# Kernel optimization log

Hardware: AMD Instinct MI355X
Metric: run time of the kernel (lower is better)

## Reference

```python
import jax, jax.numpy as jnp
import numpy as np

NUM_EXPERTS = 8
TOP_K = 2
B, L, H = 4, 4096, 1024


def setup_inputs() -> dict:
    key = jax.random.key(0)
    ks = jax.random.split(key, 5)
    s = 1.0 / np.sqrt(H)
    return {
        "hidden_states": jax.random.normal(ks[0], (B, L, H), dtype=jnp.float32),
        "gate_w": jax.random.normal(ks[1], (H, NUM_EXPERTS), dtype=jnp.float32) * s,
        "w1": jax.random.normal(ks[2], (NUM_EXPERTS, H, 2 * H), dtype=jnp.float32) * s,
        "b1": jnp.zeros((NUM_EXPERTS, 2 * H), dtype=jnp.float32),
        "w2": jax.random.normal(ks[3], (NUM_EXPERTS, 2 * H, H), dtype=jnp.float32) * (1.0 / np.sqrt(2 * H)),
        "b2": jnp.zeros((NUM_EXPERTS, H), dtype=jnp.float32),
    }


def reference(hidden_states, gate_w, w1, b1, w2, b2):
    b, l, h = hidden_states.shape
    flat = hidden_states.reshape(-1, h)                      # [T, H]
    router_logits = flat @ gate_w                            # [T, E]
    probs = jax.nn.softmax(router_logits, axis=-1)
    weights, indices = jax.lax.top_k(probs, TOP_K)           # [T, K]
    weights = weights / jnp.sum(weights, axis=-1, keepdims=True)
    # combine[t, e] = sum_k weights[t, k] * 1{indices[t, k] == e}
    onehot = jax.nn.one_hot(indices, NUM_EXPERTS, dtype=flat.dtype)  # [T, K, E]
    combine = jnp.einsum('tk,tke->te', weights, onehot)      # [T, E]
    out = jnp.zeros_like(flat)
    for e in range(NUM_EXPERTS):  # fixed small expert loop; dense-compute, sparse-combine
        hdn = jax.nn.relu(flat @ w1[e] + b1[e])              # [T, 2H]
        y = hdn @ w2[e] + b2[e]                              # [T, H]
        out = out + combine[:, e:e + 1] * y
    return out.reshape(b, l, h)
```

## Files before the change

kernel.cpp:

```cpp
#include <hip/hip_runtime.h>
#include <hip/hip_bf16.h>
#include <stdint.h>

#define T_TOK 16384
#define HD    1024
#define HD2   2048
#define NE    8
#define ROWS  (2*T_TOK)
#define MAXT  264
#define RTOK  32

#define M_NT    256
#define M_OFFS  272
#define M_TILES 288

typedef __bf16 bf16x8 __attribute__((ext_vector_type(8)));
typedef float f32x4 __attribute__((ext_vector_type(4)));
typedef float f32x16 __attribute__((ext_vector_type(16)));

#define GLD16(g, l) __builtin_amdgcn_global_load_lds( \
    (const __attribute__((address_space(1))) void*)(g), \
    (__attribute__((address_space(3))) void*)(l), 16, 0, 0)

__device__ inline unsigned short f2bf(float f) {
    unsigned int u = __float_as_uint(f);
    unsigned int r = (u + 0x7fffu + ((u >> 16) & 1u)) >> 16;
    return (unsigned short)r;
}

__global__ __launch_bounds__(256) void cvt_wT(const float* __restrict__ w,
                                              unsigned short* __restrict__ wt,
                                              int K, int N) {
    __shared__ float t[32][33];
    int e = blockIdx.z;
    int n0 = blockIdx.x * 32, k0 = blockIdx.y * 32;
    int r = threadIdx.x >> 3;
    int c4 = (threadIdx.x & 7) * 4;
    const float* src = w + ((size_t)e * K + k0 + r) * N + n0 + c4;
    float4 v = *(const float4*)src;
    t[r][c4] = v.x; t[r][c4+1] = v.y; t[r][c4+2] = v.z; t[r][c4+3] = v.w;
    __syncthreads();
    int cc = threadIdx.x & 7;
    ushort4 o;
    o.x = f2bf(t[cc*4+0][r]); o.y = f2bf(t[cc*4+1][r]);
    o.z = f2bf(t[cc*4+2][r]); o.w = f2bf(t[cc*4+3][r]);
    *(ushort4*)(wt + ((size_t)e * N + n0 + r) * K + k0 + cc*4) = o;
}

__global__ __launch_bounds__(256) void router_k(const float* __restrict__ x,
        const float* __restrict__ gw, int* __restrict__ meta,
        int* __restrict__ tok_e, int* __restrict__ tok_slot, float* __restrict__ tok_w,
        unsigned short* __restrict__ xb) {
    __shared__ float g[NE * HD];
    __shared__ int   le[RTOK * 2];
    __shared__ float lw[RTOK * 2];
    __shared__ int   lslot[RTOK * 2];
    __shared__ int   lcnt[NE];
    __shared__ int   lbase[NE];
    for (int i = threadIdx.x; i < NE * HD; i += 256) {
        int k = i >> 3, e = i & 7;
        g[e * HD + k] = gw[i];
    }
    if (threadIdx.x < NE) lcnt[threadIdx.x] = 0;
    __syncthreads();

    int wave = threadIdx.x >> 6, lane = threadIdx.x & 63;
    int t0 = blockIdx.x * RTOK;
    for (int i = 0; i < RTOK / 4; i++) {
        int tt = wave * (RTOK / 4) + i;
        int t = t0 + tt;
        const float4* xr = (const float4*)(x + (size_t)t * HD);
        float acc[NE];
#pragma unroll
        for (int e = 0; e < NE; e++) acc[e] = 0.f;
#pragma unroll
        for (int j = 0; j < HD / 256; j++) {
            float4 xv = xr[lane + 64 * j];
            ushort4 o4;
            o4.x = f2bf(xv.x); o4.y = f2bf(xv.y);
            o4.z = f2bf(xv.z); o4.w = f2bf(xv.w);
            *(ushort4*)(xb + (size_t)t * HD + (lane + 64 * j) * 4) = o4;
#pragma unroll
            for (int e = 0; e < NE; e++) {
                float4 gv = *(const float4*)&g[e * HD + (lane + 64 * j) * 4];
                acc[e] += xv.x * gv.x + xv.y * gv.y + xv.z * gv.z + xv.w * gv.w;
            }
        }
#pragma unroll
        for (int e = 0; e < NE; e++) {
            float v = acc[e];
#pragma unroll
            for (int off = 32; off > 0; off >>= 1) v += __shfl_down(v, off, 64);
            acc[e] = v;
        }
        if (lane == 0) {
            int e1 = 0; float l1 = acc[0];
#pragma unroll
            for (int e = 1; e < NE; e++) if (acc[e] > l1) { l1 = acc[e]; e1 = e; }
            int e2 = -1; float l2 = -3.0e38f;
#pragma unroll
            for (int e = 0; e < NE; e++) if (e != e1 && acc[e] > l2) { l2 = acc[e]; e2 = e; }
            float w1 = 1.f / (1.f + expf(l2 - l1));
            le[tt * 2] = e1;     le[tt * 2 + 1] = e2;
            lw[tt * 2] = w1;     lw[tt * 2 + 1] = 1.f - w1;
        }
    }
    __syncthreads();
    if (threadIdx.x < RTOK * 2)
        lslot[threadIdx.x] = atomicAdd(&lcnt[le[threadIdx.x]], 1);
    __syncthreads();
    if (threadIdx.x < NE)
        lbase[threadIdx.x] = atomicAdd(&meta[threadIdx.x * 32], lcnt[threadIdx.x]);
    __syncthreads();
    if (threadIdx.x < RTOK * 2) {
        int gi = t0 * 2 + threadIdx.x;
        int e = le[threadIdx.x];
        tok_e[gi]    = e;
        tok_slot[gi] = lbase[e] + lslot[threadIdx.x];
        tok_w[gi]    = lw[threadIdx.x];
    }
}

__global__ __launch_bounds__(64) void offsets_k(int* __restrict__ meta) {
    int lane = threadIdx.x;
    int cl = (lane < NE) ? meta[lane * 32] : 0;
    int cnt[NE], offs[NE], tbase[NE];
    int o = 0, tb = 0;
#pragma unroll
    for (int e = 0; e < NE; e++) {
        cnt[e] = __shfl(cl, e, 64);
        offs[e] = o;  o += cnt[e];
        tbase[e] = tb; tb += (cnt[e] + 127) >> 7;
    }
    int nt = tb;
    if (lane == 0) meta[M_NT] = nt;
    if (lane < NE) meta[M_OFFS + lane] = offs[lane];
    for (int i = lane; i < nt; i += 64) {
        int e = 0;
#pragma unroll
        for (int k = 1; k < NE; k++) if (i >= tbase[k]) e = k;
        int m = i - tbase[e];
        int r0 = offs[e] + m * 128;
        int re = offs[e] + cnt[e];
        if (r0 + 128 < re) re = r0 + 128;
        meta[M_TILES + i] = e;
        meta[M_TILES + MAXT + i] = r0;
        meta[M_TILES + 2 * MAXT + i] = re;
    }
}

__global__ __launch_bounds__(256) void scatter_k(const int* __restrict__ meta,
        const int* __restrict__ tok_e, const int* __restrict__ tok_slot,
        const float* __restrict__ tok_w, int* __restrict__ rows_tok,
        float* __restrict__ rows_w) {
    int i = blockIdx.x * 256 + threadIdx.x;
    const int* offs = meta + M_OFFS;
    int e = tok_e[i];
    int r = offs[e] + tok_slot[i];
    rows_tok[r] = i >> 1;
    rows_w[r] = tok_w[i];
}

__global__ __launch_bounds__(256) void gemm1_k(
    const unsigned short* __restrict__ Xbf,
    const unsigned short* __restrict__ W1T,
    const float* __restrict__ b1,
    const int* __restrict__ meta,
    const int* __restrict__ rows_tok,
    unsigned short* __restrict__ hdn)
{
    __shared__ unsigned short As[128 * 64];
    __shared__ unsigned short Bs[128 * 64];
    int nt = meta[M_NT];
    int mt = blockIdx.y;
    if (mt >= nt) return;
    int e    = meta[M_TILES + mt];
    int r0   = meta[M_TILES + MAXT + mt];
    int rend = meta[M_TILES + 2 * MAXT + mt];
    int n0 = blockIdx.x * 128;

    int tid = threadIdx.x, w = tid >> 6, lane = tid & 63;

    const unsigned short* srcA[4];
    const unsigned short* srcB[4];
#pragma unroll
    for (int j = 0; j < 4; j++) {
        int g = w * 256 + j * 64 + lane;
        int row = g >> 3;
        int c = (g & 7) ^ (row & 7);
        int grow = r0 + row; grow = grow < ROWS - 1 ? grow : ROWS - 1;
        int tok = rows_tok[grow];
        srcA[j] = Xbf + (size_t)tok * HD + c * 8;
        srcB[j] = W1T + ((size_t)e * HD2 + n0 + row) * HD + c * 8;
    }
    int wm = (w & 1) * 64, wn = (w >> 1) * 64;

    f32x4 acc[4][4];
#pragma unroll
    for (int a = 0; a < 4; a++)
#pragma unroll
        for (int b = 0; b < 4; b++) acc[a][b] = (f32x4){0.f, 0.f, 0.f, 0.f};

    for (int kt = 0; kt < HD / 64; kt++) {
        __syncthreads();
#pragma unroll
        for (int j = 0; j < 4; j++) {
            GLD16(srcA[j] + kt * 64, &As[(w * 256 + j * 64) * 8]);
            GLD16(srcB[j] + kt * 64, &Bs[(w * 256 + j * 64) * 8]);
        }
        __syncthreads();
#pragma unroll
        for (int s = 0; s < 2; s++) {
            bf16x8 af[4], bfr[4];
            int q = lane >> 4, cA = s * 4 + q;
#pragma unroll
            for (int i = 0; i < 4; i++) {
                int rowA = wm + i * 16 + (lane & 15);
                af[i] = *(const bf16x8*)&As[(rowA * 8 + (cA ^ (rowA & 7))) * 8];
                int rowB = wn + i * 16 + (lane & 15);
                bfr[i] = *(const bf16x8*)&Bs[(rowB * 8 + (cA ^ (rowB & 7))) * 8];
            }
#pragma unroll
            for (int im = 0; im < 4; im++)
#pragma unroll
                for (int in = 0; in < 4; in++)
                    acc[im][in] = __builtin_amdgcn_mfma_f32_16x16x32_bf16(
                        af[im], bfr[in], acc[im][in], 0, 0, 0);
        }
    }

    const float* b1e = b1 + (size_t)e * HD2 + n0 + wn;
    int q = lane >> 4;
#pragma unroll
    for (int in = 0; in < 4; in++) {
        float bias = b1e[in * 16 + (lane & 15)];
#pragma unroll
        for (int im = 0; im < 4; im++) {
            int rbase = r0 + wm + im * 16 + q * 4;
#pragma unroll
            for (int i = 0; i < 4; i++) {
                int r = rbase + i;
                if (r < rend) {
                    float v = acc[im][in][i] + bias;
                    v = v > 0.f ? v : 0.f;
                    hdn[(size_t)r * HD2 + n0 + wn + in * 16 + (lane & 15)] = f2bf(v);
                }
            }
        }
    }
}

__global__ __launch_bounds__(256) void gemm2_k(
    const unsigned short* __restrict__ hdn,
    const unsigned short* __restrict__ W2T,
    const float* __restrict__ b2,
    const int* __restrict__ meta,
    const int* __restrict__ rows_tok,
    const float* __restrict__ rows_w,
    float* __restrict__ out)
{
    __shared__ unsigned short As[128 * 64];
    __shared__ unsigned short Bs[128 * 64];
    int nt = meta[M_NT];
    int mt = blockIdx.y;
    if (mt >= nt) return;
    int e    = meta[M_TILES + mt];
    int r0   = meta[M_TILES + MAXT + mt];
    int rend = meta[M_TILES + 2 * MAXT + mt];
    int n0 = blockIdx.x * 128;

    int tid = threadIdx.x, w = tid >> 6, lane = tid & 63;

    const unsigned short* srcA[4];
    const unsigned short* srcB[4];
#pragma unroll
    for (int j = 0; j < 4; j++) {
        int g = w * 256 + j * 64 + lane;
        int row = g >> 3;
        int c = (g & 7) ^ (row & 7);
        int grow = r0 + row; grow = grow < ROWS - 1 ? grow : ROWS - 1;
        srcA[j] = hdn + (size_t)grow * HD2 + c * 8;
        srcB[j] = W2T + ((size_t)e * HD + n0 + row) * HD2 + c * 8;
    }
    int wm = (w & 1) * 64, wn = (w >> 1) * 64;

    f32x16 acc[2][2];
#pragma unroll
    for (int a = 0; a < 2; a++)
#pragma unroll
        for (int b = 0; b < 2; b++)
#pragma unroll
            for (int i = 0; i < 16; i++) acc[a][b][i] = 0.f;

    int kh = lane >> 5;
    int rl = lane & 31;
    for (int kt = 0; kt < HD2 / 64; kt++) {
        __syncthreads();
#pragma unroll
        for (int j = 0; j < 4; j++) {
            GLD16(srcA[j] + kt * 64, &As[(w * 256 + j * 64) * 8]);
            GLD16(srcB[j] + kt * 64, &Bs[(w * 256 + j * 64) * 8]);
        }
        __syncthreads();
#pragma unroll
        for (int s = 0; s < 4; s++) {
            int c = s * 2 + kh;
            bf16x8 af[2], bfr[2];
#pragma unroll
            for (int i = 0; i < 2; i++) {
                int rowA = wm + i * 32 + rl;
                af[i] = *(const bf16x8*)&As[(rowA * 8 + (c ^ (rowA & 7))) * 8];
                int rowB = wn + i * 32 + rl;
                bfr[i] = *(const bf16x8*)&Bs[(rowB * 8 + (c ^ (rowB & 7))) * 8];
            }
#pragma unroll
            for (int im = 0; im < 2; im++)
#pragma unroll
                for (int in = 0; in < 2; in++)
                    acc[im][in] = __builtin_amdgcn_mfma_f32_32x32x16_bf16(
                        af[im], bfr[in], acc[im][in], 0, 0, 0);
        }
    }

    int col = lane & 31;
    float bias0 = b2[(size_t)e * HD + n0 + wn + col];
    float bias1 = b2[(size_t)e * HD + n0 + wn + 32 + col];
#pragma unroll
    for (int im = 0; im < 2; im++) {
        int rb = r0 + wm + im * 32 + 4 * kh;
#pragma unroll
        for (int g = 0; g < 4; g++) {
            int toks[4]; float wgts[4];
#pragma unroll
            for (int t = 0; t < 4; t++) {
                int r = rb + 8 * g + t;
                int rc = r < ROWS - 1 ? r : ROWS - 1;
                toks[t] = rows_tok[rc];
                wgts[t] = rows_w[rc];
            }
#pragma unroll
            for (int in = 0; in < 2; in++) {
                float bias = in ? bias1 : bias0;
#pragma unroll
                for (int t = 0; t < 4; t++) {
                    int r = rb + 8 * g + t;
                    if (r < rend) {
                        float v = (acc[im][in][g * 4 + t] + bias) * wgts[t];
                        atomicAdd(&out[(size_t)toks[t] * HD + n0 + wn + in * 32 + col], v);
                    }
                }
            }
        }
    }
}

extern "C" void kernel_launch(void* const* d_in, const int* in_sizes, int n_in,
                              void* d_out, int out_size, void* d_ws, size_t ws_size,
                              hipStream_t stream) {
    const float* x  = (const float*)d_in[0];
    const float* gw = (const float*)d_in[1];
    const float* w1 = (const float*)d_in[2];
    const float* b1 = (const float*)d_in[3];
    const float* w2 = (const float*)d_in[4];
    const float* b2 = (const float*)d_in[5];
    float* out = (float*)d_out;

    uint8_t* ws = (uint8_t*)d_ws;
    unsigned short* Xbf = (unsigned short*)(ws);
    unsigned short* W1T = (unsigned short*)(ws + 33554432ull);
    unsigned short* W2T = (unsigned short*)(ws + 67108864ull);
    unsigned short* HDN = (unsigned short*)(ws + 100663296ull);
    int*   meta     = (int*)(ws + 234881024ull);
    int*   tok_e    = meta + 2048;
    int*   tok_slot = tok_e + ROWS;
    float* tok_w    = (float*)(tok_slot + ROWS);
    int*   rows_tok = (int*)(tok_w + ROWS);
    float* rows_w   = (float*)(rows_tok + ROWS);

    hipMemsetAsync(meta, 0, 1024, stream);
    hipMemsetAsync(d_out, 0, (size_t)out_size * sizeof(float), stream);

    cvt_wT<<<dim3(HD2 / 32, HD / 32, NE), 256, 0, stream>>>(w1, W1T, HD, HD2);
    cvt_wT<<<dim3(HD / 32, HD2 / 32, NE), 256, 0, stream>>>(w2, W2T, HD2, HD);
    router_k<<<T_TOK / RTOK, 256, 0, stream>>>(x, gw, meta, tok_e, tok_slot, tok_w, Xbf);
    offsets_k<<<1, 64, 0, stream>>>(meta);
    scatter_k<<<ROWS / 256, 256, 0, stream>>>(meta, tok_e, tok_slot, tok_w, rows_tok, rows_w);
    gemm1_k<<<dim3(HD2 / 128, MAXT), 256, 0, stream>>>(Xbf, W1T, b1, meta, rows_tok, HDN);
    gemm2_k<<<dim3(HD / 128, MAXT), 256, 0, stream>>>(HDN, W2T, b2, meta, rows_tok, rows_w, out);
}
```

Measured before the change: 773.5 us.

## Use 256x256 tiles with double-buffered LDS pipelining in both expert GEMMs

Both grouped GEMMs move from 128x128 tiles with 256 threads to 256x256 tiles with 512 threads and 8 waves. The main loop now double-buffers LDS and interleaves async global-to-LDS loads of the next k-tile with MFMA on the current one, using explicit waitcnt, barriers and setprio. Block indices are remapped so consecutive blocks share weight tiles, and routing tiles become 256 rows. This aims to hide memory latency and raise data reuse, at the cost of 128KB LDS per block, heavier register pressure and more padding waste on partial expert tiles.

```diff
diff --git a/kernel.cpp b/kernel.cpp
--- a/kernel.cpp
+++ b/kernel.cpp
@@ -8,6 +8,7 @@
 #define NE    8
 #define ROWS  (2*T_TOK)
 #define MAXT  264
+#define MT256 136
 #define RTOK  32
 
 #define M_NT    256
@@ -16,7 +17,6 @@
 
 typedef __bf16 bf16x8 __attribute__((ext_vector_type(8)));
 typedef float f32x4 __attribute__((ext_vector_type(4)));
-typedef float f32x16 __attribute__((ext_vector_type(16)));
 
 #define GLD16(g, l) __builtin_amdgcn_global_load_lds( \
     (const __attribute__((address_space(1))) void*)(g), \
@@ -130,7 +130,7 @@
     for (int e = 0; e < NE; e++) {
         cnt[e] = __shfl(cl, e, 64);
         offs[e] = o;  o += cnt[e];
-        tbase[e] = tb; tb += (cnt[e] + 127) >> 7;
+        tbase[e] = tb; tb += (cnt[e] + 255) >> 8;
     }
     int nt = tb;
     if (lane == 0) meta[M_NT] = nt;
@@ -140,9 +140,9 @@
 #pragma unroll
         for (int k = 1; k < NE; k++) if (i >= tbase[k]) e = k;
         int m = i - tbase[e];
-        int r0 = offs[e] + m * 128;
+        int r0 = offs[e] + m * 256;
         int re = offs[e] + cnt[e];
-        if (r0 + 128 < re) re = r0 + 128;
+        if (r0 + 256 < re) re = r0 + 256;
         meta[M_TILES + i] = e;
         meta[M_TILES + MAXT + i] = r0;
         meta[M_TILES + 2 * MAXT + i] = re;
@@ -161,7 +161,46 @@
     rows_w[r] = tok_w[i];
 }
 
-__global__ __launch_bounds__(256) void gemm1_k(
+
+#define ST_A(H, SB, KTN) do { \
+    GLD16(pa[H][0] + (KTN) * 64, &As[(SB) + ((H) * 1024 + w * 64) * 8]); \
+    GLD16(pa[H][1] + (KTN) * 64, &As[(SB) + ((H) * 1024 + 512 + w * 64) * 8]); } while (0)
+#define ST_B(H, SB, KTN) do { \
+    GLD16(pb[H][0] + (KTN) * 64, &Bs[(SB) + ((H) * 1024 + w * 64) * 8]); \
+    GLD16(pb[H][1] + (KTN) * 64, &Bs[(SB) + ((H) * 1024 + 512 + w * 64) * 8]); } while (0)
+#define LD_A(AH, RBUF) do { \
+    _Pragma("unroll") \
+    for (int im_ = 0; im_ < 4; im_++) { \
+        int row_ = (AH) * 128 + wm * 64 + im_ * 16 + rl; \
+        _Pragma("unroll") \
+        for (int ks_ = 0; ks_ < 2; ks_++) { \
+            int g_ = (ks_ * 4 + q) ^ (row_ & 7); \
+            af[im_][ks_] = *(const bf16x8*)&As[(RBUF) + row_ * 64 + g_ * 8]; \
+        } } } while (0)
+#define LD_B(DST, BH, RBUF) do { \
+    _Pragma("unroll") \
+    for (int in_ = 0; in_ < 2; in_++) { \
+        int row_ = (BH) * 128 + wn * 32 + in_ * 16 + rl; \
+        _Pragma("unroll") \
+        for (int ks_ = 0; ks_ < 2; ks_++) { \
+            int g_ = (ks_ * 4 + q) ^ (row_ & 7); \
+            DST[in_][ks_] = *(const bf16x8*)&Bs[(RBUF) + row_ * 64 + g_ * 8]; \
+        } } } while (0)
+#define MM(AH, BH, BF) do { \
+    _Pragma("unroll") \
+    for (int im_ = 0; im_ < 4; im_++) \
+    _Pragma("unroll") \
+    for (int in_ = 0; in_ < 2; in_++) \
+    _Pragma("unroll") \
+    for (int ks_ = 0; ks_ < 2; ks_++) \
+        acc[AH][BH][im_][in_] = __builtin_amdgcn_mfma_f32_16x16x32_bf16( \
+            af[im_][ks_], BF[in_][ks_], acc[AH][BH][im_][in_], 0, 0, 0); } while (0)
+#define SB0()  __builtin_amdgcn_sched_barrier(0)
+#define VMW4() do { asm volatile("s_waitcnt vmcnt(4)" ::: "memory"); SB0(); } while (0)
+#define BAR()  do { __builtin_amdgcn_s_barrier(); SB0(); } while (0)
+#define PRIO(P) __builtin_amdgcn_s_setprio(P)
+
+__global__ __launch_bounds__(512, 2) void gemm1_k(
     const unsigned short* __restrict__ Xbf,
     const unsigned short* __restrict__ W1T,
     const float* __restrict__ b1,
@@ -169,88 +208,106 @@
     const int* __restrict__ rows_tok,
     unsigned short* __restrict__ hdn)
 {
-    __shared__ unsigned short As[128 * 64];
-    __shared__ unsigned short Bs[128 * 64];
+    __shared__ unsigned short As[2 * 16384];
+    __shared__ unsigned short Bs[2 * 16384];
     int nt = meta[M_NT];
-    int mt = blockIdx.y;
+    int fid = blockIdx.y * 8 + blockIdx.x;
+    int lid = (fid & 7) * MT256 + (fid >> 3);
+    int xx = lid & 7, mt = lid >> 3;
     if (mt >= nt) return;
     int e    = meta[M_TILES + mt];
     int r0   = meta[M_TILES + MAXT + mt];
     int rend = meta[M_TILES + 2 * MAXT + mt];
-    int n0 = blockIdx.x * 128;
+    int n0 = xx * 256;
 
     int tid = threadIdx.x, w = tid >> 6, lane = tid & 63;
-
-    const unsigned short* srcA[4];
-    const unsigned short* srcB[4];
-#pragma unroll
-    for (int j = 0; j < 4; j++) {
-        int g = w * 256 + j * 64 + lane;
-        int row = g >> 3;
-        int c = (g & 7) ^ (row & 7);
-        int grow = r0 + row; grow = grow < ROWS - 1 ? grow : ROWS - 1;
-        int tok = rows_tok[grow];
-        srcA[j] = Xbf + (size_t)tok * HD + c * 8;
-        srcB[j] = W1T + ((size_t)e * HD2 + n0 + row) * HD + c * 8;
-    }
-    int wm = (w & 1) * 64, wn = (w >> 1) * 64;
-
-    f32x4 acc[4][4];
-#pragma unroll
-    for (int a = 0; a < 4; a++)
-#pragma unroll
-        for (int b = 0; b < 4; b++) acc[a][b] = (f32x4){0.f, 0.f, 0.f, 0.f};
-
+    int wm = w >> 2, wn = w & 3;
+    int rl = lane & 15, q = lane >> 4;
+
+    const unsigned short* pa[2][2];
+    const unsigned short* pb[2][2];
+#pragma unroll
+    for (int h = 0; h < 2; h++)
+#pragma unroll
+        for (int c = 0; c < 2; c++) {
+            int gg = c * 512 + tid;
+            int row = gg >> 3, cc = gg & 7, cl = cc ^ (row & 7);
+            int grow = r0 + h * 128 + row;
+            grow = grow < ROWS - 1 ? grow : ROWS - 1;
+            int tok = rows_tok[grow];
+            pa[h][c] = Xbf + (size_t)tok * HD + cl * 8;
+            pb[h][c] = W1T + ((size_t)e * HD2 + n0 + h * 128 + row) * HD + cl * 8;
+        }
+
+    f32x4 acc[2][2][4][2];
+#pragma unroll
+    for (int a = 0; a < 2; a++)
+#pragma unroll
+    for (int b = 0; b < 2; b++)
+#pragma unroll
+    for (int i = 0; i < 4; i++)
+#pragma unroll
+    for (int n = 0; n < 2; n++)
+        acc[a][b][i][n] = (f32x4){0.f, 0.f, 0.f, 0.f};
+
+    bf16x8 af[4][2], bf0[2][2], bf1[2][2];
+
+    ST_A(0, 0, 0); ST_B(0, 0, 0); ST_B(1, 0, 0); ST_A(1, 0, 0);
+    VMW4(); BAR();
+
+#pragma unroll 1
     for (int kt = 0; kt < HD / 64; kt++) {
-        __syncthreads();
-#pragma unroll
-        for (int j = 0; j < 4; j++) {
-            GLD16(srcA[j] + kt * 64, &As[(w * 256 + j * 64) * 8]);
-            GLD16(srcB[j] + kt * 64, &Bs[(w * 256 + j * 64) * 8]);
-        }
-        __syncthreads();
-#pragma unroll
-        for (int s = 0; s < 2; s++) {
-            bf16x8 af[4], bfr[4];
-            int q = lane >> 4, cA = s * 4 + q;
-#pragma unroll
-            for (int i = 0; i < 4; i++) {
-                int rowA = wm + i * 16 + (lane & 15);
-                af[i] = *(const bf16x8*)&As[(rowA * 8 + (cA ^ (rowA & 7))) * 8];
-                int rowB = wn + i * 16 + (lane & 15);
-                bfr[i] = *(const bf16x8*)&Bs[(rowB * 8 + (cA ^ (rowB & 7))) * 8];
-            }
-#pragma unroll
-            for (int im = 0; im < 4; im++)
-#pragma unroll
-                for (int in = 0; in < 4; in++)
-                    acc[im][in] = __builtin_amdgcn_mfma_f32_16x16x32_bf16(
-                        af[im], bfr[in], acc[im][in], 0, 0, 0);
-        }
-    }
-
-    const float* b1e = b1 + (size_t)e * HD2 + n0 + wn;
-    int q = lane >> 4;
-#pragma unroll
-    for (int in = 0; in < 4; in++) {
-        float bias = b1e[in * 16 + (lane & 15)];
+        int rbuf = (kt & 1) << 14;
+        int sbuf = rbuf ^ 16384;
+        int ktn = (kt + 1 < HD / 64) ? kt + 1 : HD / 64 - 1;
+        LD_A(0, rbuf); LD_B(bf0, 0, rbuf);
+        ST_A(0, sbuf, ktn);
+        VMW4(); BAR();
+        PRIO(1); MM(0, 0, bf0); PRIO(0);
+        BAR();
+        LD_B(bf1, 1, rbuf);
+        ST_B(0, sbuf, ktn);
+        VMW4(); BAR();
+        PRIO(1); MM(0, 1, bf1); PRIO(0);
+        BAR();
+        LD_A(1, rbuf);
+        ST_B(1, sbuf, ktn);
+        BAR();
+        PRIO(1); MM(1, 1, bf1); PRIO(0);
+        BAR();
+        LD_B(bf0, 0, rbuf);
+        ST_A(1, sbuf, ktn);
+        VMW4(); BAR();
+        PRIO(1); MM(1, 0, bf0); PRIO(0);
+        BAR();
+    }
+
+    const float* b1e = b1 + (size_t)e * HD2;
+#pragma unroll
+    for (int ah = 0; ah < 2; ah++)
+#pragma unroll
+    for (int bh = 0; bh < 2; bh++)
+#pragma unroll
+    for (int in = 0; in < 2; in++) {
+        int col = n0 + bh * 128 + wn * 32 + in * 16 + rl;
+        float bias = b1e[col];
 #pragma unroll
         for (int im = 0; im < 4; im++) {
-            int rbase = r0 + wm + im * 16 + q * 4;
-#pragma unroll
-            for (int i = 0; i < 4; i++) {
-                int r = rbase + i;
+            int rb2 = r0 + ah * 128 + wm * 64 + im * 16 + q * 4;
+#pragma unroll
+            for (int j = 0; j < 4; j++) {
+                int r = rb2 + j;
                 if (r < rend) {
-                    float v = acc[im][in][i] + bias;
+                    float v = acc[ah][bh][im][in][j] + bias;
                     v = v > 0.f ? v : 0.f;
-                    hdn[(size_t)r * HD2 + n0 + wn + in * 16 + (lane & 15)] = f2bf(v);
+                    hdn[(size_t)r * HD2 + col] = f2bf(v);
                 }
             }
         }
     }
 }
 
-__global__ __launch_bounds__(256) void gemm2_k(
+__global__ __launch_bounds__(512, 2) void gemm2_k(
     const unsigned short* __restrict__ hdn,
     const unsigned short* __restrict__ W2T,
     const float* __restrict__ b2,
@@ -259,95 +316,104 @@
     const float* __restrict__ rows_w,
     float* __restrict__ out)
 {
-    __shared__ unsigned short As[128 * 64];
-    __shared__ unsigned short Bs[128 * 64];
+    __shared__ unsigned short As[2 * 16384];
+    __shared__ unsigned short Bs[2 * 16384];
     int nt = meta[M_NT];
-    int mt = blockIdx.y;
+    int fid = blockIdx.y * 4 + blockIdx.x;
+    int lid = (fid & 7) * (MT256 / 2) + (fid >> 3);
+    int xx = lid & 3, mt = lid >> 2;
     if (mt >= nt) return;
     int e    = meta[M_TILES + mt];
     int r0   = meta[M_TILES + MAXT + mt];
     int rend = meta[M_TILES + 2 * MAXT + mt];
-    int n0 = blockIdx.x * 128;
+    int n0 = xx * 256;
 
     int tid = threadIdx.x, w = tid >> 6, lane = tid & 63;
-
-    const unsigned short* srcA[4];
-    const unsigned short* srcB[4];
-#pragma unroll
-    for (int j = 0; j < 4; j++) {
-        int g = w * 256 + j * 64 + lane;
-        int row = g >> 3;
-        int c = (g & 7) ^ (row & 7);
-        int grow = r0 + row; grow = grow < ROWS - 1 ? grow : ROWS - 1;
-        srcA[j] = hdn + (size_t)grow * HD2 + c * 8;
-        srcB[j] = W2T + ((size_t)e * HD + n0 + row) * HD2 + c * 8;
-    }
-    int wm = (w & 1) * 64, wn = (w >> 1) * 64;
-
-    f32x16 acc[2][2];
+    int wm = w >> 2, wn = w & 3;
+    int rl = lane & 15, q = lane >> 4;
+
+    const unsigned short* pa[2][2];
+    const unsigned short* pb[2][2];
+#pragma unroll
+    for (int h = 0; h < 2; h++)
+#pragma unroll
+        for (int c = 0; c < 2; c++) {
+            int gg = c * 512 + tid;
+            int row = gg >> 3, cc = gg & 7, cl = cc ^ (row & 7);
+            int grow = r0 + h * 128 + row;
+            grow = grow < ROWS - 1 ? grow : ROWS - 1;
+            pa[h][c] = hdn + (size_t)grow * HD2 + cl * 8;
+            pb[h][c] = W2T + ((size_t)e * HD + n0 + h * 128 + row) * HD2 + cl * 8;
+        }
+
+    f32x4 acc[2][2][4][2];
 #pragma unroll
     for (int a = 0; a < 2; a++)
 #pragma unroll
-        for (int b = 0; b < 2; b++)
-#pragma unroll
-            for (int i = 0; i < 16; i++) acc[a][b][i] = 0.f;
-
-    int kh = lane >> 5;
-    int rl = lane & 31;
+    for (int b = 0; b < 2; b++)
+#pragma unroll
+    for (int i = 0; i < 4; i++)
+#pragma unroll
+    for (int n = 0; n < 2; n++)
+        acc[a][b][i][n] = (f32x4){0.f, 0.f, 0.f, 0.f};
+
+    bf16x8 af[4][2], bf0[2][2], bf1[2][2];
+
+    ST_A(0, 0, 0); ST_B(0, 0, 0); ST_B(1, 0, 0); ST_A(1, 0, 0);
+    VMW4(); BAR();
+
+#pragma unroll 1
     for (int kt = 0; kt < HD2 / 64; kt++) {
-        __syncthreads();
+        int rbuf = (kt & 1) << 14;
+        int sbuf = rbuf ^ 16384;
+        int ktn = (kt + 1 < HD2 / 64) ? kt + 1 : HD2 / 64 - 1;
+        LD_A(0, rbuf); LD_B(bf0, 0, rbuf);
+        ST_A(0, sbuf, ktn);
+        VMW4(); BAR();
+        PRIO(1); MM(0, 0, bf0); PRIO(0);
+        BAR();
+        LD_B(bf1, 1, rbuf);
+        ST_B(0, sbuf, ktn);
+        VMW4(); BAR();
+        PRIO(1); MM(0, 1, bf1); PRIO(0);
+        BAR();
+        LD_A(1, rbuf);
+        ST_B(1, sbuf, ktn);
+        BAR();
+        PRIO(1); MM(1, 1, bf1); PRIO(0);
+        BAR();
+        LD_B(bf0, 0, rbuf);
+        ST_A(1, sbuf, ktn);
+        VMW4(); BAR();
+        PRIO(1); MM(1, 0, bf0); PRIO(0);
+        BAR();
+    }
+
+    const float* b2e = b2 + (size_t)e * HD;
+    float bias[2][2];
+#pragma unroll
+    for (int bh = 0; bh < 2; bh++)
+#pragma unroll
+        for (int in = 0; in < 2; in++)
+            bias[bh][in] = b2e[n0 + bh * 128 + wn * 32 + in * 16 + rl];
+#pragma unroll
+    for (int ah = 0; ah < 2; ah++)
+#pragma unroll
+    for (int im = 0; im < 4; im++) {
+        int rb2 = r0 + ah * 128 + wm * 64 + im * 16 + q * 4;
 #pragma unroll
         for (int j = 0; j < 4; j++) {
-            GLD16(srcA[j] + kt * 64, &As[(w * 256 + j * 64) * 8]);
-            GLD16(srcB[j] + kt * 64, &Bs[(w * 256 + j * 64) * 8]);
-        }
-        __syncthreads();
-#pragma unroll
-        for (int s = 0; s < 4; s++) {
-            int c = s * 2 + kh;
-            bf16x8 af[2], bfr[2];
-#pragma unroll
-            for (int i = 0; i < 2; i++) {
-                int rowA = wm + i * 32 + rl;
-                af[i] = *(const bf16x8*)&As[(rowA * 8 + (c ^ (rowA & 7))) * 8];
-                int rowB = wn + i * 32 + rl;
-                bfr[i] = *(const bf16x8*)&Bs[(rowB * 8 + (c ^ (rowB & 7))) * 8];
-            }
-#pragma unroll
-            for (int im = 0; im < 2; im++)
-#pragma unroll
-                for (int in = 0; in < 2; in++)
-                    acc[im][in] = __builtin_amdgcn_mfma_f32_32x32x16_bf16(
-                        af[im], bfr[in], acc[im][in], 0, 0, 0);
-        }
-    }
-
-    int col = lane & 31;
-    float bias0 = b2[(size_t)e * HD + n0 + wn + col];
-    float bias1 = b2[(size_t)e * HD + n0 + wn + 32 + col];
-#pragma unroll
-    for (int im = 0; im < 2; im++) {
-        int rb = r0 + wm + im * 32 + 4 * kh;
-#pragma unroll
-        for (int g = 0; g < 4; g++) {
-            int toks[4]; float wgts[4];
-#pragma unroll
-            for (int t = 0; t < 4; t++) {
-                int r = rb + 8 * g + t;
-                int rc = r < ROWS - 1 ? r : ROWS - 1;
-                toks[t] = rows_tok[rc];
-                wgts[t] = rows_w[rc];
-            }
-#pragma unroll
-            for (int in = 0; in < 2; in++) {
-                float bias = in ? bias1 : bias0;
-#pragma unroll
-                for (int t = 0; t < 4; t++) {
-                    int r = rb + 8 * g + t;
-                    if (r < rend) {
-                        float v = (acc[im][in][g * 4 + t] + bias) * wgts[t];
-                        atomicAdd(&out[(size_t)toks[t] * HD + n0 + wn + in * 32 + col], v);
-                    }
+            int r = rb2 + j;
+            if (r < rend) {
+                int tok = rows_tok[r];
+                float wt = rows_w[r];
+                float* op = out + (size_t)tok * HD + n0;
+#pragma unroll
+                for (int bh = 0; bh < 2; bh++)
+#pragma unroll
+                for (int in = 0; in < 2; in++) {
+                    float v = (acc[ah][bh][im][in][j] + bias[bh][in]) * wt;
+                    atomicAdd(op + bh * 128 + wn * 32 + in * 16 + rl, v);
                 }
             }
         }
@@ -385,6 +451,6 @@
     router_k<<<T_TOK / RTOK, 256, 0, stream>>>(x, gw, meta, tok_e, tok_slot, tok_w, Xbf);
     offsets_k<<<1, 64, 0, stream>>>(meta);
     scatter_k<<<ROWS / 256, 256, 0, stream>>>(meta, tok_e, tok_slot, tok_w, rows_tok, rows_w);
-    gemm1_k<<<dim3(HD2 / 128, MAXT), 256, 0, stream>>>(Xbf, W1T, b1, meta, rows_tok, HDN);
-    gemm2_k<<<dim3(HD / 128, MAXT), 256, 0, stream>>>(HDN, W2T, b2, meta, rows_tok, rows_w, out);
-}
+    gemm1_k<<<dim3(HD2 / 256, MT256), 512, 0, stream>>>(Xbf, W1T, b1, meta, rows_tok, HDN);
+    gemm2_k<<<dim3(HD / 256, MT256), 512, 0, stream>>>(HDN, W2T, b2, meta, rows_tok, rows_w, out);
+}
```

Result: slower. 794.7 us (+2.7%).
